# Optimization experiments

Measured on AMD Instinct MI355X. Metric: run time of the kernel, lower is better.

## Reference

```python
import jax, jax.numpy as jnp
import numpy as np

H = 8       # n_heads
N = 128     # n_vars
HEAD = 64   # per-head dim (== __init__ dim)


def setup_inputs() -> dict:
    key = jax.random.key(0)
    k0, k1, k2, k3, k4 = jax.random.split(key, 5)
    B, L = 4, 8192
    D = H * HEAD
    x = jax.random.normal(k0, (B, L, D), dtype=jnp.float32)
    # nn.Linear default init: U(-1/sqrt(fan_in), 1/sqrt(fan_in)), fan_in = HEAD
    s = 1.0 / np.sqrt(HEAD)
    w1 = jax.random.uniform(k1, (HEAD, HEAD), jnp.float32, -s, s)
    b1 = jax.random.uniform(k2, (HEAD,), jnp.float32, -s, s)
    w2 = jax.random.uniform(k3, (HEAD, HEAD), jnp.float32, -s, s)
    b2 = jax.random.uniform(k4, (HEAD,), jnp.float32, -s, s)
    return {"x": x, "w1": w1, "b1": b1, "w2": w2, "b2": b2}


def reference(x, w1, b1, w2, b2):
    B, L, D = x.shape
    P = L // N  # patches per variable
    # (B,L,D) -> (B,H,L,HEAD) -> (B,H,N,P,HEAD)
    xh = x.reshape(B, L, H, HEAD).transpose(0, 2, 1, 3).reshape(B, H, N, P, HEAD)
    q = xh @ w1.T + b1  # proj_1
    k = xh @ w2.T + b2  # proj_2
    # per (b,h,patch) NxN adjacency over variables
    adj = jax.nn.gelu(jnp.einsum('bhixd,bhjxd->bhxij', q, k), approximate=False)
    adj = jax.nn.softmax(adj, axis=-1)
    # dropout is identity in eval mode; F.normalize(p=1): divide by max(L1, eps)
    adj = adj / jnp.maximum(jnp.sum(jnp.abs(adj), axis=-1, keepdims=True), 1e-12)
    out = jnp.einsum('bhxij,bhjxd->bixhd', adj, xh)  # (B,N,P,H,HEAD)
    return out.reshape(B, L, H * HEAD)
```

## Files before the change

### kernel.cpp

```cpp
#include <hip/hip_runtime.h>
#include <math.h>


namespace {
constexpr int H = 8, NV = 128, HEAD = 64, B = 4, L = 8192;
constexpr int P = L / NV;
constexpr int D = H * HEAD;
constexpr int RS = P * D;

constexpr int XT_S = 136;
constexpr int QK_S = 72;
constexpr int A_S  = 136;

typedef _Float16 half8  __attribute__((ext_vector_type(8)));
typedef _Float16 half4v __attribute__((ext_vector_type(4)));
typedef _Float16 half2v __attribute__((ext_vector_type(2)));
typedef float    floatx4 __attribute__((ext_vector_type(4)));

__device__ __forceinline__ floatx4 mfma16(half8 a, half8 b, floatx4 c) {
    return __builtin_amdgcn_mfma_f32_16x16x32_f16(a, b, c, 0, 0, 0);
}

__device__ __forceinline__ half8 cvt8(float4 a, float4 b) {
    half8 r;
    r[0]=(_Float16)a.x; r[1]=(_Float16)a.y; r[2]=(_Float16)a.z; r[3]=(_Float16)a.w;
    r[4]=(_Float16)b.x; r[5]=(_Float16)b.y; r[6]=(_Float16)b.z; r[7]=(_Float16)b.w;
    return r;
}

__global__ __launch_bounds__(256) void pack_w(const float4* __restrict__ w1,
                                              const float4* __restrict__ w2,
                                              half4v* __restrict__ wh) {
    const int t = blockIdx.x * 256 + threadIdx.x;
    const float4 a = w1[t];
    const float4 b = w2[t];
    half4v ha, hb;
    ha[0]=(_Float16)a.x; ha[1]=(_Float16)a.y; ha[2]=(_Float16)a.z; ha[3]=(_Float16)a.w;
    hb[0]=(_Float16)b.x; hb[1]=(_Float16)b.y; hb[2]=(_Float16)b.z; hb[3]=(_Float16)b.w;
    wh[t] = ha;
    wh[1024 + t] = hb;
}

__global__ __launch_bounds__(256, 3) void space_graph_mfma3(
    const float* __restrict__ x, const _Float16* __restrict__ wh,
    const float* __restrict__ b1, const float* __restrict__ b2,
    float* __restrict__ out)
{
    __shared__ _Float16 lds[64 * XT_S + 2 * NV * QK_S];
    _Float16* Xt = lds;
    _Float16* Qh = lds + 64 * XT_S;
    _Float16* Kh = Qh + NV * QK_S;
    _Float16* A  = Qh;

    const int t    = threadIdx.x;
    const int lane = t & 63;
    const int w    = t >> 6;
    const int col  = lane & 15;
    const int quad = lane >> 4;

    const int blk = blockIdx.x;
    const int p = blk & (P - 1);
    const int h = (blk >> 6) & (H - 1);
    const int b = blk >> 9;
    const size_t base = ((size_t)b * L + (size_t)p) * D + (size_t)h * HEAD;

    {
        const int c  = t & 15;
        const int tt = t >> 4;
        #pragma unroll
        for (int it = 0; it < 4; ++it) {
            const int j0 = 2 * (tt + 16 * it);
            const float4 v0 = *(const float4*)(x + base + (size_t)j0 * RS + c * 4);
            const float4 v1 = *(const float4*)(x + base + (size_t)(j0 + 1) * RS + c * 4);
            const float va[4] = {v0.x, v0.y, v0.z, v0.w};
            const float vb[4] = {v1.x, v1.y, v1.z, v1.w};
            #pragma unroll
            for (int q = 0; q < 4; ++q) {
                half2v pr; pr[0] = (_Float16)va[q]; pr[1] = (_Float16)vb[q];
                *(half2v*)&Xt[(4 * c + q) * XT_S + j0] = pr;
            }
        }
    }

    floatx4 qacc[2][4], kacc[2][4];
    #pragma unroll
    for (int mt = 0; mt < 2; ++mt)
        #pragma unroll
        for (int nt = 0; nt < 4; ++nt) { qacc[mt][nt] = (floatx4)0.0f; kacc[mt][nt] = (floatx4)0.0f; }

    half8 axf[2][2];
    #pragma unroll
    for (int mt = 0; mt < 2; ++mt)
        #pragma unroll
        for (int ks = 0; ks < 2; ++ks) {
            const int row = 32 * w + 16 * mt + col;
            const float* src = x + base + (size_t)row * RS + quad * 8 + 32 * ks;
            axf[mt][ks] = cvt8(*(const float4*)src, *(const float4*)(src + 4));
        }

    const _Float16* w1h = wh;
    const _Float16* w2h = wh + HEAD * HEAD;
    #pragma unroll
    for (int ks = 0; ks < 2; ++ks)
        #pragma unroll
        for (int nt = 0; nt < 4; ++nt) {
            const int n = col + 16 * nt, k0 = quad * 8 + 32 * ks;
            const half8 wb1 = *(const half8*)&w1h[n * HEAD + k0];
            const half8 wb2 = *(const half8*)&w2h[n * HEAD + k0];
            #pragma unroll
            for (int mt = 0; mt < 2; ++mt) {
                qacc[mt][nt] = mfma16(axf[mt][ks], wb1, qacc[mt][nt]);
                kacc[mt][nt] = mfma16(axf[mt][ks], wb2, kacc[mt][nt]);
            }
        }

    float bb1[4], bb2[4];
    #pragma unroll
    for (int nt = 0; nt < 4; ++nt) { bb1[nt] = b1[col + 16 * nt]; bb2[nt] = b2[col + 16 * nt]; }
    #pragma unroll
    for (int mt = 0; mt < 2; ++mt)
        #pragma unroll
        for (int r = 0; r < 4; ++r) {
            const int R = 32 * w + 16 * mt + quad * 4 + r;
            _Float16* qrow = &Qh[R * QK_S + col];
            _Float16* krow = &Kh[R * QK_S + col];
            #pragma unroll
            for (int nt = 0; nt < 4; ++nt) {
                qrow[nt * 16] = (_Float16)(qacc[mt][nt][r] + bb1[nt]);
                krow[nt * 16] = (_Float16)(kacc[mt][nt][r] + bb2[nt]);
            }
        }
    __syncthreads();

    floatx4 sacc[2][8];
    #pragma unroll
    for (int mt = 0; mt < 2; ++mt)
        #pragma unroll
        for (int nt = 0; nt < 8; ++nt) sacc[mt][nt] = (floatx4)0.0f;

    #pragma unroll
    for (int ks = 0; ks < 2; ++ks) {
        half8 qaf[2];
        #pragma unroll
        for (int mt = 0; mt < 2; ++mt)
            qaf[mt] = *(const half8*)&Qh[(32 * w + 16 * mt + col) * QK_S + quad * 8 + 32 * ks];
        #pragma unroll
        for (int nt = 0; nt < 8; ++nt) {
            const half8 kbf = *(const half8*)&Kh[(col + 16 * nt) * QK_S + quad * 8 + 32 * ks];
            #pragma unroll
            for (int mt = 0; mt < 2; ++mt)
                sacc[mt][nt] = mfma16(qaf[mt], kbf, sacc[mt][nt]);
        }
    }
    __syncthreads();

    #pragma unroll
    for (int mt = 0; mt < 2; ++mt)
        #pragma unroll
        for (int r = 0; r < 4; ++r) {
            float wv[8]; float rs = 0.f;
            #pragma unroll
            for (int nt = 0; nt < 8; ++nt) {
                const float s  = sacc[mt][nt][r];
                const float u  = s * fmaf(s * s, 0.035677408137f, 0.7978845608f);
                const float em = __expf(-2.0f * u);
                const float g  = s * __builtin_amdgcn_rcpf(1.0f + em);
                const float e  = __expf(g);
                wv[nt] = e; rs += e;
            }
            rs += __shfl_xor(rs, 1); rs += __shfl_xor(rs, 2);
            rs += __shfl_xor(rs, 4); rs += __shfl_xor(rs, 8);
            const float inv = __builtin_amdgcn_rcpf(rs);
            const int R = 32 * w + 16 * mt + quad * 4 + r;
            _Float16* arow = &A[R * A_S + col];
            #pragma unroll
            for (int nt = 0; nt < 8; ++nt)
                arow[nt * 16] = (_Float16)(wv[nt] * inv);
        }

    floatx4 oacc[2][4];
    #pragma unroll
    for (int mt = 0; mt < 2; ++mt)
        #pragma unroll
        for (int nt = 0; nt < 4; ++nt) oacc[mt][nt] = (floatx4)0.0f;

    #pragma unroll
    for (int ks = 0; ks < 4; ++ks) {
        half8 aaf[2];
        #pragma unroll
        for (int mt = 0; mt < 2; ++mt)
            aaf[mt] = *(const half8*)&A[(32 * w + 16 * mt + col) * A_S + quad * 8 + 32 * ks];
        #pragma unroll
        for (int nt = 0; nt < 4; ++nt) {
            const half8 xbf = *(const half8*)&Xt[(col + 16 * nt) * XT_S + quad * 8 + 32 * ks];
            #pragma unroll
            for (int mt = 0; mt < 2; ++mt)
                oacc[mt][nt] = mfma16(aaf[mt], xbf, oacc[mt][nt]);
        }
    }

    #pragma unroll
    for (int mt = 0; mt < 2; ++mt)
        #pragma unroll
        for (int r = 0; r < 4; ++r) {
            const int i = 32 * w + 16 * mt + quad * 4 + r;
            float* orow = out + base + (size_t)i * RS + col;
            #pragma unroll
            for (int nt = 0; nt < 4; ++nt)
                orow[nt * 16] = oacc[mt][nt][r];
        }
}
}

extern "C" void kernel_launch(void* const* d_in, const int* in_sizes, int n_in,
                              void* d_out, int out_size, void* d_ws, size_t ws_size,
                              hipStream_t stream) {
    const float* x  = (const float*)d_in[0];
    const float* w1 = (const float*)d_in[1];
    const float* b1 = (const float*)d_in[2];
    const float* w2 = (const float*)d_in[3];
    const float* b2 = (const float*)d_in[4];
    float* out = (float*)d_out;
    _Float16* wh = (_Float16*)d_ws;

    hipLaunchKernelGGL(pack_w, dim3(4), dim3(256), 0, stream,
                       (const float4*)w1, (const float4*)w2, (half4v*)wh);
    hipLaunchKernelGGL(space_graph_mfma3, dim3(B * H * P), dim3(256), 0, stream,
                       x, wh, b1, b2, out);
}
```

Measured before the change: 148.7 us.

## Use 512-thread blocks with one 16-row tile per wave and vectorized output stores

Doubles the block to 8 waves so each wave owns a single 16-row M tile instead of two, halving per-wave accumulator registers and raising occupancy bounds. The final AV product is transposed (X^T as the A operand, adjacency as B) so that each lane holds 4 contiguous output columns and can write float4 stores instead of scalar ones. It adds more waves contending for the same LDS and reduces per-wave MFMA reuse of the loaded B fragments.

```diff
diff --git a/kernel.cpp b/kernel.cpp
--- a/kernel.cpp
+++ b/kernel.cpp
@@ -41,7 +41,7 @@
     wh[1024 + t] = hb;
 }
 
-__global__ __launch_bounds__(256, 3) void space_graph_mfma3(
+__global__ __launch_bounds__(512, 6) void space_graph_mfma4(
     const float* __restrict__ x, const _Float16* __restrict__ wh,
     const float* __restrict__ b1, const float* __restrict__ b2,
     float* __restrict__ out)
@@ -68,8 +68,8 @@
         const int c  = t & 15;
         const int tt = t >> 4;
         #pragma unroll
-        for (int it = 0; it < 4; ++it) {
-            const int j0 = 2 * (tt + 16 * it);
+        for (int it = 0; it < 2; ++it) {
+            const int j0 = 2 * tt + 64 * it;
             const float4 v0 = *(const float4*)(x + base + (size_t)j0 * RS + c * 4);
             const float4 v1 = *(const float4*)(x + base + (size_t)(j0 + 1) * RS + c * 4);
             const float va[4] = {v0.x, v0.y, v0.z, v0.w};
@@ -82,21 +82,17 @@
         }
     }
 
-    floatx4 qacc[2][4], kacc[2][4];
-    #pragma unroll
-    for (int mt = 0; mt < 2; ++mt)
-        #pragma unroll
-        for (int nt = 0; nt < 4; ++nt) { qacc[mt][nt] = (floatx4)0.0f; kacc[mt][nt] = (floatx4)0.0f; }
-
-    half8 axf[2][2];
-    #pragma unroll
-    for (int mt = 0; mt < 2; ++mt)
-        #pragma unroll
-        for (int ks = 0; ks < 2; ++ks) {
-            const int row = 32 * w + 16 * mt + col;
-            const float* src = x + base + (size_t)row * RS + quad * 8 + 32 * ks;
-            axf[mt][ks] = cvt8(*(const float4*)src, *(const float4*)(src + 4));
-        }
+    floatx4 qacc[4], kacc[4];
+    #pragma unroll
+    for (int nt = 0; nt < 4; ++nt) { qacc[nt] = (floatx4)0.0f; kacc[nt] = (floatx4)0.0f; }
+
+    half8 axf[2];
+    #pragma unroll
+    for (int ks = 0; ks < 2; ++ks) {
+        const int row = 16 * w + col;
+        const float* src = x + base + (size_t)row * RS + quad * 8 + 32 * ks;
+        axf[ks] = cvt8(*(const float4*)src, *(const float4*)(src + 4));
+    }
 
     const _Float16* w1h = wh;
     const _Float16* w2h = wh + HEAD * HEAD;
@@ -107,108 +103,83 @@
             const int n = col + 16 * nt, k0 = quad * 8 + 32 * ks;
             const half8 wb1 = *(const half8*)&w1h[n * HEAD + k0];
             const half8 wb2 = *(const half8*)&w2h[n * HEAD + k0];
-            #pragma unroll
-            for (int mt = 0; mt < 2; ++mt) {
-                qacc[mt][nt] = mfma16(axf[mt][ks], wb1, qacc[mt][nt]);
-                kacc[mt][nt] = mfma16(axf[mt][ks], wb2, kacc[mt][nt]);
-            }
-        }
-
-    float bb1[4], bb2[4];
-    #pragma unroll
-    for (int nt = 0; nt < 4; ++nt) { bb1[nt] = b1[col + 16 * nt]; bb2[nt] = b2[col + 16 * nt]; }
-    #pragma unroll
-    for (int mt = 0; mt < 2; ++mt)
-        #pragma unroll
-        for (int r = 0; r < 4; ++r) {
-            const int R = 32 * w + 16 * mt + quad * 4 + r;
-            _Float16* qrow = &Qh[R * QK_S + col];
-            _Float16* krow = &Kh[R * QK_S + col];
-            #pragma unroll
-            for (int nt = 0; nt < 4; ++nt) {
-                qrow[nt * 16] = (_Float16)(qacc[mt][nt][r] + bb1[nt]);
-                krow[nt * 16] = (_Float16)(kacc[mt][nt][r] + bb2[nt]);
-            }
-        }
+            qacc[nt] = mfma16(axf[ks], wb1, qacc[nt]);
+            kacc[nt] = mfma16(axf[ks], wb2, kacc[nt]);
+        }
+
+    #pragma unroll
+    for (int r = 0; r < 4; ++r) {
+        const int R = 16 * w + quad * 4 + r;
+        _Float16* qrow = &Qh[R * QK_S + col];
+        _Float16* krow = &Kh[R * QK_S + col];
+        #pragma unroll
+        for (int nt = 0; nt < 4; ++nt) {
+            qrow[nt * 16] = (_Float16)(qacc[nt][r] + b1[col + 16 * nt]);
+            krow[nt * 16] = (_Float16)(kacc[nt][r] + b2[col + 16 * nt]);
+        }
+    }
     __syncthreads();
 
-    floatx4 sacc[2][8];
-    #pragma unroll
-    for (int mt = 0; mt < 2; ++mt)
-        #pragma unroll
-        for (int nt = 0; nt < 8; ++nt) sacc[mt][nt] = (floatx4)0.0f;
+    floatx4 sacc[8];
+    #pragma unroll
+    for (int nt = 0; nt < 8; ++nt) sacc[nt] = (floatx4)0.0f;
 
     #pragma unroll
     for (int ks = 0; ks < 2; ++ks) {
-        half8 qaf[2];
-        #pragma unroll
-        for (int mt = 0; mt < 2; ++mt)
-            qaf[mt] = *(const half8*)&Qh[(32 * w + 16 * mt + col) * QK_S + quad * 8 + 32 * ks];
+        const half8 qaf = *(const half8*)&Qh[(16 * w + col) * QK_S + quad * 8 + 32 * ks];
         #pragma unroll
         for (int nt = 0; nt < 8; ++nt) {
             const half8 kbf = *(const half8*)&Kh[(col + 16 * nt) * QK_S + quad * 8 + 32 * ks];
-            #pragma unroll
-            for (int mt = 0; mt < 2; ++mt)
-                sacc[mt][nt] = mfma16(qaf[mt], kbf, sacc[mt][nt]);
+            sacc[nt] = mfma16(qaf, kbf, sacc[nt]);
         }
     }
     __syncthreads();
 
     #pragma unroll
-    for (int mt = 0; mt < 2; ++mt)
-        #pragma unroll
-        for (int r = 0; r < 4; ++r) {
-            float wv[8]; float rs = 0.f;
-            #pragma unroll
-            for (int nt = 0; nt < 8; ++nt) {
-                const float s  = sacc[mt][nt][r];
-                const float u  = s * fmaf(s * s, 0.035677408137f, 0.7978845608f);
-                const float em = __expf(-2.0f * u);
-                const float g  = s * __builtin_amdgcn_rcpf(1.0f + em);
-                const float e  = __expf(g);
-                wv[nt] = e; rs += e;
-            }
-            rs += __shfl_xor(rs, 1); rs += __shfl_xor(rs, 2);
-            rs += __shfl_xor(rs, 4); rs += __shfl_xor(rs, 8);
-            const float inv = __builtin_amdgcn_rcpf(rs);
-            const int R = 32 * w + 16 * mt + quad * 4 + r;
-            _Float16* arow = &A[R * A_S + col];
-            #pragma unroll
-            for (int nt = 0; nt < 8; ++nt)
-                arow[nt * 16] = (_Float16)(wv[nt] * inv);
-        }
-
-    floatx4 oacc[2][4];
-    #pragma unroll
-    for (int mt = 0; mt < 2; ++mt)
-        #pragma unroll
-        for (int nt = 0; nt < 4; ++nt) oacc[mt][nt] = (floatx4)0.0f;
+    for (int r = 0; r < 4; ++r) {
+        float wv[8]; float rs = 0.f;
+        #pragma unroll
+        for (int nt = 0; nt < 8; ++nt) {
+            const float s  = sacc[nt][r];
+            const float u  = s * fmaf(s * s, 0.035677408137f, 0.7978845608f);
+            const float em = __expf(-2.0f * u);
+            const float g  = s * __builtin_amdgcn_rcpf(1.0f + em);
+            const float e  = __expf(g);
+            wv[nt] = e; rs += e;
+        }
+        rs += __shfl_xor(rs, 1); rs += __shfl_xor(rs, 2);
+        rs += __shfl_xor(rs, 4); rs += __shfl_xor(rs, 8);
+        const float inv = __builtin_amdgcn_rcpf(rs);
+        const int R = 16 * w + quad * 4 + r;
+        _Float16* arow = &A[R * A_S + col];
+        #pragma unroll
+        for (int nt = 0; nt < 8; ++nt)
+            arow[nt * 16] = (_Float16)(wv[nt] * inv);
+    }
+
+    floatx4 oacc[4];
+    #pragma unroll
+    for (int mt = 0; mt < 4; ++mt) oacc[mt] = (floatx4)0.0f;
 
     #pragma unroll
     for (int ks = 0; ks < 4; ++ks) {
-        half8 aaf[2];
-        #pragma unroll
-        for (int mt = 0; mt < 2; ++mt)
-            aaf[mt] = *(const half8*)&A[(32 * w + 16 * mt + col) * A_S + quad * 8 + 32 * ks];
-        #pragma unroll
-        for (int nt = 0; nt < 4; ++nt) {
-            const half8 xbf = *(const half8*)&Xt[(col + 16 * nt) * XT_S + quad * 8 + 32 * ks];
-            #pragma unroll
-            for (int mt = 0; mt < 2; ++mt)
-                oacc[mt][nt] = mfma16(aaf[mt], xbf, oacc[mt][nt]);
-        }
-    }
-
-    #pragma unroll
-    for (int mt = 0; mt < 2; ++mt)
-        #pragma unroll
-        for (int r = 0; r < 4; ++r) {
-            const int i = 32 * w + 16 * mt + quad * 4 + r;
-            float* orow = out + base + (size_t)i * RS + col;
-            #pragma unroll
-            for (int nt = 0; nt < 4; ++nt)
-                orow[nt * 16] = oacc[mt][nt][r];
-        }
+        const half8 bf = *(const half8*)&A[(16 * w + col) * A_S + quad * 8 + 32 * ks];
+        #pragma unroll
+        for (int mt = 0; mt < 4; ++mt) {
+            const half8 af = *(const half8*)&Xt[(16 * mt + col) * XT_S + quad * 8 + 32 * ks];
+            oacc[mt] = mfma16(af, bf, oacc[mt]);
+        }
+    }
+
+    {
+        const size_t rowoff = base + (size_t)(16 * w + col) * RS + quad * 4;
+        #pragma unroll
+        for (int mt = 0; mt < 4; ++mt) {
+            float4 v; v.x = oacc[mt][0]; v.y = oacc[mt][1];
+            v.z = oacc[mt][2]; v.w = oacc[mt][3];
+            *(float4*)(out + rowoff + 16 * mt) = v;
+        }
+    }
 }
 }
 
@@ -225,6 +196,6 @@
 
     hipLaunchKernelGGL(pack_w, dim3(4), dim3(256), 0, stream,
                        (const float4*)w1, (const float4*)w2, (half4v*)wh);
-    hipLaunchKernelGGL(space_graph_mfma3, dim3(B * H * P), dim3(256), 0, stream,
+    hipLaunchKernelGGL(space_graph_mfma4, dim3(B * H * P), dim3(512), 0, stream,
                        x, wh, b1, b2, out);
 }
```

After: 172.3 us. 1.16x slower.

## Transpose output MFMA so each lane writes float4 rows; use exp2 in GELU-softmax

Applied to the files above, without the earlier changes.

The final A·X MFMA is reformulated as X^T·A^T, so each lane's accumulator holds 4 contiguous head-dim values of one output row. That lets the epilogue issue float4 global stores instead of scalar strided stores. The GELU/softmax arithmetic is rewritten with exp2 and prescaled constants, and results are kept in the score registers. The barrier is moved to after the softmax so it overlaps with the K reads. The main aim is to cut the number of store instructions and improve write coalescing, at the cost of a slightly different register layout.

```diff
diff --git a/kernel.cpp b/kernel.cpp
--- a/kernel.cpp
+++ b/kernel.cpp
@@ -41,7 +41,7 @@
     wh[1024 + t] = hb;
 }
 
-__global__ __launch_bounds__(256, 3) void space_graph_mfma3(
+__global__ __launch_bounds__(256, 3) void space_graph_mfma5(
     const float* __restrict__ x, const _Float16* __restrict__ wh,
     const float* __restrict__ b1, const float* __restrict__ b2,
     float* __restrict__ out)
@@ -152,63 +152,72 @@
                 sacc[mt][nt] = mfma16(qaf[mt], kbf, sacc[mt][nt]);
         }
     }
-    __syncthreads();
 
     #pragma unroll
     for (int mt = 0; mt < 2; ++mt)
         #pragma unroll
         for (int r = 0; r < 4; ++r) {
-            float wv[8]; float rs = 0.f;
+            float rs = 0.f;
             #pragma unroll
             for (int nt = 0; nt < 8; ++nt) {
                 const float s  = sacc[mt][nt][r];
-                const float u  = s * fmaf(s * s, 0.035677408137f, 0.7978845608f);
-                const float em = __expf(-2.0f * u);
-                const float g  = s * __builtin_amdgcn_rcpf(1.0f + em);
-                const float e  = __expf(g);
-                wv[nt] = e; rs += e;
+                const float a  = s * fmaf(s * s, -0.1029534f, -2.3022083f);
+                const float em = __builtin_amdgcn_exp2f(a);
+                const float g2 = (s * 1.44269504089f) * __builtin_amdgcn_rcpf(1.0f + em);
+                const float e  = __builtin_amdgcn_exp2f(g2);
+                sacc[mt][nt][r] = e; rs += e;
             }
             rs += __shfl_xor(rs, 1); rs += __shfl_xor(rs, 2);
             rs += __shfl_xor(rs, 4); rs += __shfl_xor(rs, 8);
             const float inv = __builtin_amdgcn_rcpf(rs);
+            #pragma unroll
+            for (int nt = 0; nt < 8; ++nt) sacc[mt][nt][r] *= inv;
+        }
+
+    __syncthreads();
+
+    #pragma unroll
+    for (int mt = 0; mt < 2; ++mt)
+        #pragma unroll
+        for (int r = 0; r < 4; ++r) {
             const int R = 32 * w + 16 * mt + quad * 4 + r;
             _Float16* arow = &A[R * A_S + col];
             #pragma unroll
             for (int nt = 0; nt < 8; ++nt)
-                arow[nt * 16] = (_Float16)(wv[nt] * inv);
-        }
-
-    floatx4 oacc[2][4];
-    #pragma unroll
-    for (int mt = 0; mt < 2; ++mt)
-        #pragma unroll
-        for (int nt = 0; nt < 4; ++nt) oacc[mt][nt] = (floatx4)0.0f;
+                arow[nt * 16] = (_Float16)sacc[mt][nt][r];
+        }
+
+    floatx4 oacc[4][2];
+    #pragma unroll
+    for (int mt = 0; mt < 4; ++mt)
+        #pragma unroll
+        for (int nt = 0; nt < 2; ++nt) oacc[mt][nt] = (floatx4)0.0f;
 
     #pragma unroll
     for (int ks = 0; ks < 4; ++ks) {
-        half8 aaf[2];
-        #pragma unroll
-        for (int mt = 0; mt < 2; ++mt)
-            aaf[mt] = *(const half8*)&A[(32 * w + 16 * mt + col) * A_S + quad * 8 + 32 * ks];
-        #pragma unroll
-        for (int nt = 0; nt < 4; ++nt) {
-            const half8 xbf = *(const half8*)&Xt[(col + 16 * nt) * XT_S + quad * 8 + 32 * ks];
-            #pragma unroll
-            for (int mt = 0; mt < 2; ++mt)
-                oacc[mt][nt] = mfma16(aaf[mt], xbf, oacc[mt][nt]);
-        }
-    }
-
-    #pragma unroll
-    for (int mt = 0; mt < 2; ++mt)
-        #pragma unroll
-        for (int r = 0; r < 4; ++r) {
-            const int i = 32 * w + 16 * mt + quad * 4 + r;
-            float* orow = out + base + (size_t)i * RS + col;
-            #pragma unroll
-            for (int nt = 0; nt < 4; ++nt)
-                orow[nt * 16] = oacc[mt][nt][r];
-        }
+        half8 bf[2];
+        #pragma unroll
+        for (int nt = 0; nt < 2; ++nt)
+            bf[nt] = *(const half8*)&A[(32 * w + 16 * nt + col) * A_S + quad * 8 + 32 * ks];
+        #pragma unroll
+        for (int mt = 0; mt < 4; ++mt) {
+            const half8 af = *(const half8*)&Xt[(16 * mt + col) * XT_S + quad * 8 + 32 * ks];
+            #pragma unroll
+            for (int nt = 0; nt < 2; ++nt)
+                oacc[mt][nt] = mfma16(af, bf[nt], oacc[mt][nt]);
+        }
+    }
+
+    #pragma unroll
+    for (int nt = 0; nt < 2; ++nt) {
+        const size_t rowoff = base + (size_t)(32 * w + 16 * nt + col) * RS + quad * 4;
+        #pragma unroll
+        for (int mt = 0; mt < 4; ++mt) {
+            float4 v; v.x = oacc[mt][nt][0]; v.y = oacc[mt][nt][1];
+            v.z = oacc[mt][nt][2]; v.w = oacc[mt][nt][3];
+            *(float4*)(out + rowoff + 16 * mt) = v;
+        }
+    }
 }
 }
 
@@ -225,6 +234,6 @@
 
     hipLaunchKernelGGL(pack_w, dim3(4), dim3(256), 0, stream,
                        (const float4*)w1, (const float4*)w2, (half4v*)wh);
-    hipLaunchKernelGGL(space_graph_mfma3, dim3(B * H * P), dim3(256), 0, stream,
+    hipLaunchKernelGGL(space_graph_mfma5, dim3(B * H * P), dim3(256), 0, stream,
                        x, wh, b1, b2, out);
 }
```

Measured after the change: 150.5 us. Within noise of the previous version (+1.2%).
